# Optimization experiments

Measured on AMD Instinct MI355X. Metric: run time of the kernel, lower is better.

## Reference

```python
import jax, jax.numpy as jnp
import numpy as np

B, N, D, M, H = 8, 576, 512, 16, 8
DH = D // H
K = int(D * 0.1)  # sparsity_ratio=0.1 -> k=51
EPS = 1e-5


def setup_inputs() -> dict:
    key = jax.random.key(0)
    ks = jax.random.split(key, 12)
    s = 0.02
    return {
        "F_clean": jax.random.normal(ks[0], (B, N, D), jnp.float32),
        "in_proj_w": jax.random.normal(ks[1], (3 * D, D), jnp.float32) * s,
        "in_proj_b": jnp.zeros((3 * D,), jnp.float32),
        "out_proj_w": jax.random.normal(ks[2], (D, D), jnp.float32) * s,
        "out_proj_b": jnp.zeros((D,), jnp.float32),
        "w1": jax.random.normal(ks[3], (D, D), jnp.float32) * s,
        "b1": jnp.zeros((D,), jnp.float32),
        "ln_g": jnp.ones((D,), jnp.float32),
        "ln_b": jnp.zeros((D,), jnp.float32),
        "w2": jax.random.normal(ks[4], (M, D), jnp.float32) * s,
        "b2": jnp.zeros((M,), jnp.float32),
        "templates": jax.random.normal(ks[5], (M, D), jnp.float32),
    }


def reference(F_clean, in_proj_w, in_proj_b, out_proj_w, out_proj_b,
              w1, b1, ln_g, ln_b, w2, b2, templates):
    # --- self attention (torch MultiheadAttention, batch_first, eval mode) ---
    qkv = F_clean @ in_proj_w.T + in_proj_b              # [B,N,3D]
    q, k_, v = jnp.split(qkv, 3, axis=-1)
    def heads(t):
        return t.reshape(B, N, H, DH).transpose(0, 2, 1, 3)  # [B,H,N,dh]
    q, k_, v = heads(q), heads(k_), heads(v)
    scores = jnp.einsum('bhqd,bhkd->bhqk', q, k_) / jnp.sqrt(jnp.float32(DH))
    attn = jax.nn.softmax(scores, axis=-1)
    o = jnp.einsum('bhqk,bhkd->bhqd', attn, v).transpose(0, 2, 1, 3).reshape(B, N, D)
    attn_out = o @ out_proj_w.T + out_proj_b

    F_enh = F_clean + attn_out

    # --- decompose_mlp: Linear -> LayerNorm -> GELU(exact) -> Linear ---
    h = F_enh @ w1.T + b1
    mu = jnp.mean(h, axis=-1, keepdims=True)
    var = jnp.var(h, axis=-1, keepdims=True)
    h = (h - mu) / jnp.sqrt(var + EPS) * ln_g + ln_b
    h = jax.nn.gelu(h, approximate=False)
    components = h @ w2.T + b2                           # [B,N,M]

    # --- outer product: Q[b,n,d,m] = F[b,n,d] * templates[m,d] * comp[b,n,m] ---
    Q = F_clean[:, :, :, None] * templates.T[None, None, :, :] * components[:, :, None, :]

    # --- top-k sparsify along D for each (b,n,m) row ---
    Qr = Q.transpose(0, 1, 3, 2).reshape(B * N * M, D)
    _, topk_idx = jax.lax.top_k(jnp.abs(Qr), K)
    rows = jnp.arange(B * N * M)[:, None]
    mask = jnp.zeros_like(Qr).at[rows, topk_idx].set(1.0)
    Q_sparse = (Qr * mask).reshape(B, N, M, D).transpose(0, 1, 3, 2)
    return Q_sparse
```

## Files before the change

### kernel.cpp

```cpp
#include <hip/hip_runtime.h>
#include <math.h>

#define NNB   576
#define BNR   4608
#define KSEL  51

typedef unsigned short u16;
typedef __attribute__((ext_vector_type(8))) short bf16x8;
typedef __attribute__((ext_vector_type(4))) float f32x4;

__device__ __forceinline__ u16 f2bf(float f) {
    unsigned u = __float_as_uint(f);
    return (u16)((u + 0x8000u) >> 16);
}
__device__ __forceinline__ unsigned pack2(float a, float b) {
    unsigned ua = __float_as_uint(a), ub = __float_as_uint(b);
    return ((ua + 0x8000u) >> 16) | ((ub + 0x8000u) & 0xffff0000u);
}
__device__ __forceinline__ void load_lds16(const void* gp, void* lp) {
    __builtin_amdgcn_global_load_lds((const __attribute__((address_space(1))) void*)gp,
                                     (__attribute__((address_space(3))) void*)lp, 16, 0, 0);
}
__device__ __forceinline__ float dpp_red_add_f(float x) {
    x += __int_as_float(__builtin_amdgcn_update_dpp(0, __float_as_int(x), 0x111, 0xf, 0xf, true));
    x += __int_as_float(__builtin_amdgcn_update_dpp(0, __float_as_int(x), 0x112, 0xf, 0xf, true));
    x += __int_as_float(__builtin_amdgcn_update_dpp(0, __float_as_int(x), 0x114, 0xf, 0xf, true));
    x += __int_as_float(__builtin_amdgcn_update_dpp(0, __float_as_int(x), 0x118, 0xf, 0xf, true));
    x += __int_as_float(__builtin_amdgcn_update_dpp(0, __float_as_int(x), 0x142, 0xa, 0xf, true));
    x += __int_as_float(__builtin_amdgcn_update_dpp(0, __float_as_int(x), 0x143, 0xc, 0xf, true));
    return __int_as_float(__builtin_amdgcn_readlane(__float_as_int(x), 63));
}
__device__ __forceinline__ int wave_cnt(bool p) {
    return __popcll(__ballot(p));
}

__global__ __launch_bounds__(256)
void cast_bf16(const float* __restrict__ F, const float* __restrict__ ipw,
               const float* __restrict__ opw, const float* __restrict__ w1,
               u16* __restrict__ Fb, u16* __restrict__ ipwb,
               u16* __restrict__ opwb, u16* __restrict__ w1b)
{
    size_t i4 = ((size_t)blockIdx.x * 256 + threadIdx.x) * 4;
    const float* src; u16* dst; size_t off;
    if      (i4 < 2359296) { src = F;   dst = Fb;   off = i4; }
    else if (i4 < 3145728) { src = ipw; dst = ipwb; off = i4 - 2359296; }
    else if (i4 < 3407872) { src = opw; dst = opwb; off = i4 - 3145728; }
    else                   { src = w1;  dst = w1b;  off = i4 - 3407872; }
    float4 v = *(const float4*)(src + off);
    uint2 o; o.x = pack2(v.x, v.y); o.y = pack2(v.z, v.w);
    *(uint2*)(dst + off) = o;
}

template<bool RESID, bool OUT_BF16, bool QSCALE>
__global__ __launch_bounds__(256)
void gemm_mfma64(const u16* __restrict__ A, const u16* __restrict__ Bw,
                 const float* __restrict__ bias, const float* __restrict__ res,
                 void* __restrict__ Cv, int Mr, int Nc, int Kd)
{
    __shared__ uint4 As4[512];
    __shared__ uint4 Bs4[1024];
    const int tid = threadIdx.x;
    const int lane = tid & 63, w = tid >> 6;
    const int wu = __builtin_amdgcn_readfirstlane(w);
    const int r16 = lane & 15, quad = lane >> 4;
    const int r0 = blockIdx.y << 6, c0 = blockIdx.x << 7;

    const u16* pA[2]; const u16* pB[4];
    #pragma unroll
    for (int rd = 0; rd < 2; ++rd) {
        const int c = (rd << 8) + tid;
        const int kb = c >> 8, g = (c >> 6) & 3, rr = (c >> 2) & 15, q = c & 3;
        pA[rd] = A + (size_t)(r0 + (g << 4) + rr) * Kd + (kb << 5) + (q << 3);
    }
    #pragma unroll
    for (int rd = 0; rd < 4; ++rd) {
        const int c = (rd << 8) + tid;
        const int kb = c >> 9, g = (c >> 6) & 7, rr = (c >> 2) & 15, q = c & 3;
        pB[rd] = Bw + (size_t)(c0 + (g << 4) + rr) * Kd + (kb << 5) + (q << 3);
    }

    f32x4 acc[4][2];
    #pragma unroll
    for (int i = 0; i < 4; ++i)
        #pragma unroll
        for (int j = 0; j < 2; ++j) acc[i][j] = (f32x4){0.f, 0.f, 0.f, 0.f};

    for (int kk = 0; kk < Kd; kk += 64) {
        __syncthreads();
        #pragma unroll
        for (int rd = 0; rd < 2; ++rd)
            load_lds16(pA[rd] + kk, (void*)(As4 + (rd << 8) + (wu << 6)));
        #pragma unroll
        for (int rd = 0; rd < 4; ++rd)
            load_lds16(pB[rd] + kk, (void*)(Bs4 + (rd << 8) + (wu << 6)));
        __syncthreads();
        #pragma unroll
        for (int kb = 0; kb < 2; ++kb) {
            bf16x8 af[4], bfr[2];
            #pragma unroll
            for (int i = 0; i < 4; ++i)
                af[i] = *(const bf16x8*)&As4[((kb * 4 + i) << 6) + (r16 << 2) + quad];
            #pragma unroll
            for (int j = 0; j < 2; ++j)
                bfr[j] = *(const bf16x8*)&Bs4[((kb * 8 + (w << 1) + j) << 6) + (r16 << 2) + quad];
            #pragma unroll
            for (int i = 0; i < 4; ++i)
                #pragma unroll
                for (int j = 0; j < 2; ++j)
                    acc[i][j] = __builtin_amdgcn_mfma_f32_16x16x32_bf16(af[i], bfr[j], acc[i][j], 0, 0, 0);
        }
    }

    float bcol[2], scl[2];
    #pragma unroll
    for (int j = 0; j < 2; ++j) {
        const int col = c0 + (w << 5) + (j << 4) + r16;
        bcol[j] = bias[col];
        scl[j] = (QSCALE && col < 512) ? 0.180336880111120426f : 1.0f;
    }
    #pragma unroll
    for (int i = 0; i < 4; ++i) {
        #pragma unroll
        for (int reg = 0; reg < 4; ++reg) {
            const int row = r0 + (i << 4) + (quad << 2) + reg;
            const size_t base = (size_t)row * Nc;
            #pragma unroll
            for (int j = 0; j < 2; ++j) {
                const int col = c0 + (w << 5) + (j << 4) + r16;
                float v = acc[i][j][reg] + bcol[j];
                if (RESID) v += res[base + col];
                if (QSCALE) v *= scl[j];
                if (OUT_BF16) ((u16*)Cv)[base + col] = f2bf(v);
                else          ((float*)Cv)[base + col] = v;
            }
        }
    }
}

template<bool RESID, bool OUT_BF16>
__global__ __launch_bounds__(256)
void gemm_6464(const u16* __restrict__ A, const u16* __restrict__ Bw,
               const float* __restrict__ bias, const float* __restrict__ res,
               void* __restrict__ Cv, int Mr, int Nc, int Kd)
{
    __shared__ uint4 As4[512];
    __shared__ uint4 Bs4[512];
    const int tid = threadIdx.x;
    const int lane = tid & 63, w = tid >> 6;
    const int wu = __builtin_amdgcn_readfirstlane(w);
    const int r16 = lane & 15, quad = lane >> 4;
    const int wy = w >> 1, wx = w & 1;
    const int r0 = blockIdx.y << 6, c0 = blockIdx.x << 6;

    const u16* pA[2]; const u16* pB[2];
    #pragma unroll
    for (int rd = 0; rd < 2; ++rd) {
        const int c = (rd << 8) + tid;
        const int kb = c >> 8, g = (c >> 6) & 3, rr = (c >> 2) & 15, q = c & 3;
        const int row = (g << 4) + rr;
        const int koff = (kb << 5) + (q << 3);
        pA[rd] = A  + (size_t)(r0 + row) * Kd + koff;
        pB[rd] = Bw + (size_t)(c0 + row) * Kd + koff;
    }

    f32x4 acc[2][2];
    #pragma unroll
    for (int i = 0; i < 2; ++i)
        #pragma unroll
        for (int j = 0; j < 2; ++j) acc[i][j] = (f32x4){0.f, 0.f, 0.f, 0.f};

    for (int kk = 0; kk < Kd; kk += 64) {
        __syncthreads();
        #pragma unroll
        for (int rd = 0; rd < 2; ++rd) {
            load_lds16(pA[rd] + kk, (void*)(As4 + (rd << 8) + (wu << 6)));
            load_lds16(pB[rd] + kk, (void*)(Bs4 + (rd << 8) + (wu << 6)));
        }
        __syncthreads();
        #pragma unroll
        for (int kb = 0; kb < 2; ++kb) {
            bf16x8 af[2], bfr[2];
            #pragma unroll
            for (int i = 0; i < 2; ++i)
                af[i] = *(const bf16x8*)&As4[((kb * 4 + (wy << 1) + i) << 6) + (r16 << 2) + quad];
            #pragma unroll
            for (int j = 0; j < 2; ++j)
                bfr[j] = *(const bf16x8*)&Bs4[((kb * 4 + (wx << 1) + j) << 6) + (r16 << 2) + quad];
            #pragma unroll
            for (int i = 0; i < 2; ++i)
                #pragma unroll
                for (int j = 0; j < 2; ++j)
                    acc[i][j] = __builtin_amdgcn_mfma_f32_16x16x32_bf16(af[i], bfr[j], acc[i][j], 0, 0, 0);
        }
    }

    float bcol[2];
    #pragma unroll
    for (int j = 0; j < 2; ++j) bcol[j] = bias[c0 + (wx << 5) + (j << 4) + r16];
    #pragma unroll
    for (int i = 0; i < 2; ++i) {
        #pragma unroll
        for (int reg = 0; reg < 4; ++reg) {
            const int row = r0 + (wy << 5) + (i << 4) + (quad << 2) + reg;
            const size_t base = (size_t)row * Nc;
            #pragma unroll
            for (int j = 0; j < 2; ++j) {
                const int col = c0 + (wx << 5) + (j << 4) + r16;
                float v = acc[i][j][reg] + bcol[j];
                if (RESID) v += res[base + col];
                if (OUT_BF16) ((u16*)Cv)[base + col] = f2bf(v);
                else          ((float*)Cv)[base + col] = v;
            }
        }
    }
}

__global__ __launch_bounds__(256)
void attn_mfma(const u16* __restrict__ qkv, u16* __restrict__ obuf)
{
    __shared__ uint4 Qf[512];
    __shared__ uint4 Kf[512];
    __shared__ u16  Vfs[4096];
    __shared__ u16  Pfs[4096];
    const int tid = threadIdx.x;
    const int lane = tid & 63, w = tid >> 6;
    const int wu = __builtin_amdgcn_readfirstlane(w);
    const int r16 = lane & 15, quad = lane >> 4;
    const int b = blockIdx.y >> 3, h = blockIdx.y & 7;
    const int i0 = blockIdx.x << 6;
    const u16* qb = qkv + (size_t)b * NNB * 1536 + h * 64;

    #pragma unroll
    for (int s = 0; s < 2; ++s) {
        const int linear = (s << 8) + tid;
        const int r = linear >> 3, q7 = linear & 7;
        uint4 v = *(const uint4*)(qb + (size_t)(i0 + r) * 1536 + (q7 << 3));
        Qf[(((q7 >> 2) * 4 + (r >> 4)) << 6) + ((r & 15) << 2) + (q7 & 3)] = v;
    }
    const u16* pK[2];
    #pragma unroll
    for (int rd = 0; rd < 2; ++rd) {
        const int c = (rd << 8) + tid;
        const int kb = c >> 8, g = (c >> 6) & 3, rr = (c >> 2) & 15, q = c & 3;
        pK[rd] = qb + 512 + (size_t)((g << 4) + rr) * 1536 + (kb << 5) + (q << 3);
    }
    const int vp = tid >> 3, vq7 = tid & 7;
    const int vj = vp << 1;
    const int vjl2 = (vj & 7) >> 1, vjq = (vj >> 3) & 3, vjkb = vj >> 5;

    float l_i[4] = {0.f, 0.f, 0.f, 0.f};
    f32x4 accO[4];
    #pragma unroll
    for (int f = 0; f < 4; ++f) accO[f] = (f32x4){0.f, 0.f, 0.f, 0.f};

    for (int j0 = 0; j0 < NNB; j0 += 64) {
        const u16* vbase = qb + 1024 + (size_t)(j0 + vj) * 1536 + (vq7 << 3);
        uint4 vA = *(const uint4*)vbase;
        uint4 vB = *(const uint4*)(vbase + 1536);
        __syncthreads();
        load_lds16(pK[0] + (size_t)j0 * 1536, (void*)(Kf + (wu << 6)));
        load_lds16(pK[1] + (size_t)j0 * 1536, (void*)(Kf + 256 + (wu << 6)));
        {
            const u16* ea = (const u16*)&vA;
            const u16* eb = (const u16*)&vB;
            unsigned* V32 = (unsigned*)Vfs;
            #pragma unroll
            for (int e = 0; e < 8; ++e) {
                const int d = (vq7 << 3) + e;
                const int g = d >> 4;
                const int ch = ((vjkb * 4 + g) << 6) + ((((d & 15) << 2) + vjq) ^ g);
                V32[(ch << 2) + vjl2] = (unsigned)ea[e] | ((unsigned)eb[e] << 16);
            }
        }
        __syncthreads();

        f32x4 accS[4];
        #pragma unroll
        for (int f = 0; f < 4; ++f) accS[f] = (f32x4){0.f, 0.f, 0.f, 0.f};
        #pragma unroll
        for (int kb = 0; kb < 2; ++kb) {
            bf16x8 aq = *(const bf16x8*)&Qf[((kb * 4 + w) << 6) + (r16 << 2) + quad];
            #pragma unroll
            for (int f = 0; f < 4; ++f) {
                bf16x8 bk = *(const bf16x8*)&Kf[((kb * 4 + f) << 6) + (r16 << 2) + quad];
                accS[f] = __builtin_amdgcn_mfma_f32_16x16x32_bf16(aq, bk, accS[f], 0, 0, 0);
            }
        }
        #pragma unroll
        for (int reg = 0; reg < 4; ++reg) {
            const float s0 = exp2f(accS[0][reg]);
            const float s1 = exp2f(accS[1][reg]);
            const float s2 = exp2f(accS[2][reg]);
            const float s3 = exp2f(accS[3][reg]);
            l_i[reg] += (s0 + s1) + (s2 + s3);
            const int m = (quad << 2) + reg;
            const int sm = ((m & 3) << 2) + (m >> 2);
            const float pv[4] = {s0, s1, s2, s3};
            #pragma unroll
            for (int f = 0; f < 4; ++f) {
                const int k = (f << 4) + r16;
                const int ch = (((k >> 5) * 4 + w) << 6) + (((k >> 3) & 3) << 4) + sm;
                Pfs[(ch << 3) + (k & 7)] = f2bf(pv[f]);
            }
        }
        #pragma unroll
        for (int kb = 0; kb < 2; ++kb) {
            bf16x8 ap = *(const bf16x8*)&Pfs[((((kb * 4 + w) << 6) + (quad << 4) + ((r16 & 3) << 2) + (r16 >> 2)) << 3)];
            #pragma unroll
            for (int f = 0; f < 4; ++f) {
                bf16x8 bv = *(const bf16x8*)&Vfs[((((kb * 4 + f) << 6) + (((r16 << 2) + quad) ^ f)) << 3)];
                accO[f] = __builtin_amdgcn_mfma_f32_16x16x32_bf16(ap, bv, accO[f], 0, 0, 0);
            }
        }
    }
    #pragma unroll
    for (int reg = 0; reg < 4; ++reg) {
        float l = l_i[reg];
        l += __shfl_xor(l, 1); l += __shfl_xor(l, 2);
        l += __shfl_xor(l, 4); l += __shfl_xor(l, 8);
        const float inv = 1.0f / l;
        const size_t row = (size_t)(b * NNB + i0 + (w << 4) + (quad << 2) + reg);
        #pragma unroll
        for (int f = 0; f < 4; ++f)
            obuf[row * 512 + (h << 6) + (f << 4) + r16] = f2bf(accO[f][reg] * inv);
    }
}

__global__ __launch_bounds__(256)
void outer_topk(const float* __restrict__ F, const float* __restrict__ hraw,
                const float* __restrict__ lng, const float* __restrict__ lnb,
                const float* __restrict__ w2, const float* __restrict__ b2,
                const float* __restrict__ T, float* __restrict__ out)
{
    const int bn = blockIdx.x;
    const int tid = threadIdx.x;
    const int lane = tid & 63, w = tid >> 6;
    __shared__ float Fr[512];
    __shared__ float Hr[512];
    __shared__ unsigned keyslots[4][4][64];
    __shared__ float redsm[8];

    if (tid < 128)
        *(float4*)&Fr[tid << 2] = *(const float4*)(F + (size_t)bn * 512 + (tid << 2));
    const float* hp = hraw + (size_t)bn * 512;
    float x0 = hp[tid], x1 = hp[tid + 256];
    float sw = dpp_red_add_f(x0 + x1);
    float sqw = dpp_red_add_f(x0 * x0 + x1 * x1);
    if (lane == 0) { redsm[w] = sw; redsm[4 + w] = sqw; }
    __syncthreads();
    const float s  = redsm[0] + redsm[1] + redsm[2] + redsm[3];
    const float sq = redsm[4] + redsm[5] + redsm[6] + redsm[7];
    const float mean = s * (1.0f / 512.0f);
    const float var  = sq * (1.0f / 512.0f) - mean * mean;
    const float rstd = rsqrtf(var + 1e-5f);
    float y = (x0 - mean) * rstd * lng[tid] + lnb[tid];
    Hr[tid] = 0.5f * y * (1.0f + erff(y * 0.70710678118654752f));
    y = (x1 - mean) * rstd * lng[tid + 256] + lnb[tid + 256];
    Hr[tid + 256] = 0.5f * y * (1.0f + erff(y * 0.70710678118654752f));
    __syncthreads();

    const int m0 = w << 2;
    float cm[4];
    #pragma unroll
    for (int mi = 0; mi < 4; ++mi) {
        const float* w2p = w2 + (size_t)(m0 + mi) * 512;
        float p = 0.f;
        #pragma unroll
        for (int t = 0; t < 8; ++t) p += Hr[lane + (t << 6)] * w2p[lane + (t << 6)];
        cm[mi] = dpp_red_add_f(p) + b2[m0 + mi];
    }

    unsigned u[4][8]; unsigned smask[4];
    #pragma unroll
    for (int mi = 0; mi < 4; ++mi) {
        smask[mi] = 0u;
        const float* Tp = T + (size_t)(m0 + mi) * 512;
        #pragma unroll
        for (int t = 0; t < 8; ++t) {
            float pp = Fr[lane + (t << 6)] * Tp[lane + (t << 6)];
            float pc = pp * cm[mi];
            const unsigned bits = __float_as_uint(pc);
            u[mi][t] = bits & 0x7fffffffu;
            smask[mi] |= (bits >> 31) << t;
        }
    }

    unsigned pref[4] = {0u, 0u, 0u, 0u};
    int cntP[4] = {512, 512, 512, 512};
    int U[4] = {0, 0, 0, 0};
    for (int bit = 30; bit >= 23; --bit) {
        const unsigned msk = 1u << bit;
        #pragma unroll
        for (int mi = 0; mi < 4; ++mi) {
            const unsigned cand = pref[mi] | msk;
            int cnt = 0;
            #pragma unroll
            for (int t = 0; t < 8; ++t) cnt += wave_cnt(u[mi][t] >= cand);
            if (cnt >= KSEL) { pref[mi] = cand; cntP[mi] = cnt; }
            else U[mi] = cnt;
        }
    }
    int blo[4];
    #pragma unroll
    for (int mi = 0; mi < 4; ++mi) {
        int b = 23;
        while ((cntP[mi] - U[mi]) > 64 && b > 0) {
            --b;
            const unsigned cand = pref[mi] | (1u << b);
            int cnt = 0;
            #pragma unroll
            for (int t = 0; t < 8; ++t) cnt += wave_cnt(u[mi][t] >= cand);
            if (cnt >= KSEL) { pref[mi] = cand; cntP[mi] = cnt; } else U[mi] = cnt;
        }
        blo[mi] = b;
    }
    int need[4]; bool done[4];
    #pragma unroll
    for (int mi = 0; mi < 4; ++mi) {
        need[mi] = KSEL - U[mi];
        done[mi] = (need[mi] == cntP[mi] - U[mi]);
    }

    const unsigned long long lmask = (1ull << lane) - 1ull;
    unsigned kv[4] = {0u, 0u, 0u, 0u};
    #pragma unroll
    for (int mi = 0; mi < 4; ++mi) {
        if (done[mi]) continue;
        keyslots[w][mi][lane] = 0u;
        const int bl = blo[mi];
        const unsigned lowmask = (1u << bl) - 1u;
        int running = 0;
        #pragma unroll
        for (int t = 0; t < 8; ++t) {
            const bool tie = ((u[mi][t] ^ pref[mi]) >> bl) == 0u;
            const unsigned long long M = __ballot(tie);
            const int slot = running + __popcll(M & lmask);
            if (tie && slot < 64) {
                const unsigned key = ((u[mi][t] & lowmask) << 9) | (unsigned)(511 - ((t << 6) + lane));
                keyslots[w][mi][slot] = key;
            }
            running += __popcll(M);
        }
        kv[mi] = keyslots[w][mi][lane];
    }

    unsigned prefk[4] = {0u, 0u, 0u, 0u};
    for (int bb = 31; bb >= 0; --bb) {
        if (done[0] & done[1] & done[2] & done[3]) break;
        #pragma unroll
        for (int mi = 0; mi < 4; ++mi) {
            if (done[mi]) continue;
            const unsigned candk = prefk[mi] | (1u << bb);
            const int c = __popcll(__ballot(kv[mi] >= candk));
            if (c >= need[mi]) {
                prefk[mi] = candk;
                if (c == need[mi]) done[mi] = true;
            }
        }
    }

    float* ob = out + (size_t)bn * 8192 + m0;
    #pragma unroll
    for (int t = 0; t < 8; ++t) {
        const int d = (t << 6) + lane;
        float4 v;
        float* vv = &v.x;
        #pragma unroll
        for (int mi = 0; mi < 4; ++mi) {
            const unsigned uu = u[mi][t];
            const int bl = blo[mi];
            const bool tie = ((uu ^ pref[mi]) >> bl) == 0u;
            const unsigned key = ((uu & ((1u << bl) - 1u)) << 9) | (unsigned)(511 - d);
            const bool sel = (uu >= pref[mi] + (1u << bl)) || (tie && key >= prefk[mi]);
            const unsigned bits = uu | (((smask[mi] >> t) & 1u) << 31);
            vv[mi] = sel ? __uint_as_float(bits) : 0.0f;
        }
        *(float4*)(ob + (size_t)d * 16) = v;
    }
}

extern "C" void kernel_launch(void* const* d_in, const int* in_sizes, int n_in,
                              void* d_out, int out_size, void* d_ws, size_t ws_size,
                              hipStream_t stream)
{
    const float* F    = (const float*)d_in[0];
    const float* ipw  = (const float*)d_in[1];
    const float* ipb  = (const float*)d_in[2];
    const float* opw  = (const float*)d_in[3];
    const float* opb  = (const float*)d_in[4];
    const float* w1   = (const float*)d_in[5];
    const float* b1   = (const float*)d_in[6];
    const float* lng  = (const float*)d_in[7];
    const float* lnb  = (const float*)d_in[8];
    const float* w2   = (const float*)d_in[9];
    const float* b2   = (const float*)d_in[10];
    const float* tmpl = (const float*)d_in[11];

    char* wsb = (char*)d_ws;
    u16*   qkvb  = (u16*)wsb;
    u16*   obufb = (u16*)(wsb + 14155776);
    u16*   fenhb = (u16*)(wsb + 18874368);
    float* hbuf  = (float*)(wsb + 23592960);
    u16*   Fbf   = (u16*)(wsb + 33030144);
    u16*   ipwbf = (u16*)(wsb + 37748736);
    u16*   opwbf = (u16*)(wsb + 39321600);
    u16*   w1bf  = (u16*)(wsb + 39845888);

    cast_bf16<<<3584, 256, 0, stream>>>(F, ipw, opw, w1, Fbf, ipwbf, opwbf, w1bf);
    gemm_mfma64<false, true, true><<<dim3(12, 72), 256, 0, stream>>>(Fbf, ipwbf, ipb, nullptr, qkvb, BNR, 1536, 512);
    attn_mfma<<<dim3(9, 64), 256, 0, stream>>>(qkvb, obufb);
    gemm_6464<true, true><<<dim3(8, 72), 256, 0, stream>>>(obufb, opwbf, opb, F, fenhb, BNR, 512, 512);
    gemm_6464<false, false><<<dim3(8, 72), 256, 0, stream>>>(fenhb, w1bf, b1, nullptr, hbuf, BNR, 512, 512);
    outer_topk<<<4608, 256, 0, stream>>>(F, hbuf, lng, lnb, w2, b2, tmpl, (float*)d_out);
}
```

Baseline: 289.4 us.

## Double-buffer LDS tiles in both MFMA GEMM kernels

Both bf16 MFMA GEMM kernels now keep two LDS buffers for the A and B tiles. The next K-slice's global-to-LDS loads are issued before computing on the current slice, and one barrier per iteration replaces the previous two. This is meant to overlap global memory latency with MFMA work. In exchange it doubles LDS use per block, which may reduce occupancy, and correctness relies on the barrier waiting for the async LDS loads to finish.

```diff
diff --git a/kernel.cpp b/kernel.cpp
--- a/kernel.cpp
+++ b/kernel.cpp
@@ -57,8 +57,8 @@
                  const float* __restrict__ bias, const float* __restrict__ res,
                  void* __restrict__ Cv, int Mr, int Nc, int Kd)
 {
-    __shared__ uint4 As4[512];
-    __shared__ uint4 Bs4[1024];
+    __shared__ uint4 As4[2][512];
+    __shared__ uint4 Bs4[2][1024];
     const int tid = threadIdx.x;
     const int lane = tid & 63, w = tid >> 6;
     const int wu = __builtin_amdgcn_readfirstlane(w);
@@ -85,30 +85,44 @@
         #pragma unroll
         for (int j = 0; j < 2; ++j) acc[i][j] = (f32x4){0.f, 0.f, 0.f, 0.f};
 
+    #pragma unroll
+    for (int rd = 0; rd < 2; ++rd)
+        load_lds16(pA[rd], (void*)(&As4[0][(rd << 8) + (wu << 6)]));
+    #pragma unroll
+    for (int rd = 0; rd < 4; ++rd)
+        load_lds16(pB[rd], (void*)(&Bs4[0][(rd << 8) + (wu << 6)]));
+    __syncthreads();
+
+    int cur = 0;
     for (int kk = 0; kk < Kd; kk += 64) {
-        __syncthreads();
-        #pragma unroll
-        for (int rd = 0; rd < 2; ++rd)
-            load_lds16(pA[rd] + kk, (void*)(As4 + (rd << 8) + (wu << 6)));
-        #pragma unroll
-        for (int rd = 0; rd < 4; ++rd)
-            load_lds16(pB[rd] + kk, (void*)(Bs4 + (rd << 8) + (wu << 6)));
-        __syncthreads();
+        const int nxt = kk + 64;
+        if (nxt < Kd) {
+            #pragma unroll
+            for (int rd = 0; rd < 2; ++rd)
+                load_lds16(pA[rd] + nxt, (void*)(&As4[cur ^ 1][(rd << 8) + (wu << 6)]));
+            #pragma unroll
+            for (int rd = 0; rd < 4; ++rd)
+                load_lds16(pB[rd] + nxt, (void*)(&Bs4[cur ^ 1][(rd << 8) + (wu << 6)]));
+        }
+        const uint4* Ab = As4[cur];
+        const uint4* Bb = Bs4[cur];
         #pragma unroll
         for (int kb = 0; kb < 2; ++kb) {
             bf16x8 af[4], bfr[2];
             #pragma unroll
             for (int i = 0; i < 4; ++i)
-                af[i] = *(const bf16x8*)&As4[((kb * 4 + i) << 6) + (r16 << 2) + quad];
+                af[i] = *(const bf16x8*)&Ab[((kb * 4 + i) << 6) + (r16 << 2) + quad];
             #pragma unroll
             for (int j = 0; j < 2; ++j)
-                bfr[j] = *(const bf16x8*)&Bs4[((kb * 8 + (w << 1) + j) << 6) + (r16 << 2) + quad];
+                bfr[j] = *(const bf16x8*)&Bb[((kb * 8 + (w << 1) + j) << 6) + (r16 << 2) + quad];
             #pragma unroll
             for (int i = 0; i < 4; ++i)
                 #pragma unroll
                 for (int j = 0; j < 2; ++j)
                     acc[i][j] = __builtin_amdgcn_mfma_f32_16x16x32_bf16(af[i], bfr[j], acc[i][j], 0, 0, 0);
         }
+        __syncthreads();
+        cur ^= 1;
     }
 
     float bcol[2], scl[2];
@@ -143,8 +157,8 @@
                const float* __restrict__ bias, const float* __restrict__ res,
                void* __restrict__ Cv, int Mr, int Nc, int Kd)
 {
-    __shared__ uint4 As4[512];
-    __shared__ uint4 Bs4[512];
+    __shared__ uint4 As4[2][512];
+    __shared__ uint4 Bs4[2][512];
     const int tid = threadIdx.x;
     const int lane = tid & 63, w = tid >> 6;
     const int wu = __builtin_amdgcn_readfirstlane(w);
@@ -169,29 +183,42 @@
         #pragma unroll
         for (int j = 0; j < 2; ++j) acc[i][j] = (f32x4){0.f, 0.f, 0.f, 0.f};
 
+    #pragma unroll
+    for (int rd = 0; rd < 2; ++rd) {
+        load_lds16(pA[rd], (void*)(&As4[0][(rd << 8) + (wu << 6)]));
+        load_lds16(pB[rd], (void*)(&Bs4[0][(rd << 8) + (wu << 6)]));
+    }
+    __syncthreads();
+
+    int cur = 0;
     for (int kk = 0; kk < Kd; kk += 64) {
-        __syncthreads();
-        #pragma unroll
-        for (int rd = 0; rd < 2; ++rd) {
-            load_lds16(pA[rd] + kk, (void*)(As4 + (rd << 8) + (wu << 6)));
-            load_lds16(pB[rd] + kk, (void*)(Bs4 + (rd << 8) + (wu << 6)));
-        }
-        __syncthreads();
+        const int nxt = kk + 64;
+        if (nxt < Kd) {
+            #pragma unroll
+            for (int rd = 0; rd < 2; ++rd) {
+                load_lds16(pA[rd] + nxt, (void*)(&As4[cur ^ 1][(rd << 8) + (wu << 6)]));
+                load_lds16(pB[rd] + nxt, (void*)(&Bs4[cur ^ 1][(rd << 8) + (wu << 6)]));
+            }
+        }
+        const uint4* Ab = As4[cur];
+        const uint4* Bb = Bs4[cur];
         #pragma unroll
         for (int kb = 0; kb < 2; ++kb) {
             bf16x8 af[2], bfr[2];
             #pragma unroll
             for (int i = 0; i < 2; ++i)
-                af[i] = *(const bf16x8*)&As4[((kb * 4 + (wy << 1) + i) << 6) + (r16 << 2) + quad];
+                af[i] = *(const bf16x8*)&Ab[((kb * 4 + (wy << 1) + i) << 6) + (r16 << 2) + quad];
             #pragma unroll
             for (int j = 0; j < 2; ++j)
-                bfr[j] = *(const bf16x8*)&Bs4[((kb * 4 + (wx << 1) + j) << 6) + (r16 << 2) + quad];
+                bfr[j] = *(const bf16x8*)&Bb[((kb * 4 + (wx << 1) + j) << 6) + (r16 << 2) + quad];
             #pragma unroll
             for (int i = 0; i < 2; ++i)
                 #pragma unroll
                 for (int j = 0; j < 2; ++j)
                     acc[i][j] = __builtin_amdgcn_mfma_f32_16x16x32_bf16(af[i], bfr[j], acc[i][j], 0, 0, 0);
         }
+        __syncthreads();
+        cur ^= 1;
     }
 
     float bcol[2];
```

Measured after the change: 293.2 us. About the same (+1.3%).
